# Kernel tuning notes

Hardware: AMD Instinct MI355X
Metric: run time of the kernel (lower is better)

The kernel has to match this reference:

```python
import jax, jax.numpy as jnp
import numpy as np

N_NODES = 100000
N_EDGES = 1600000
IN_CH, HID_CH, OUT_CH = 128, 128, 64
N_GRAPHS = 64


def gcn_conv(x, src, dst, W, b, n_nodes):
    """PyG-style GCNConv: self-loops already included in (src, dst).
    out_i = b + sum_j norm_ij * (x_j @ W), norm_ij = deg_i^-1/2 * deg_j^-1/2."""
    xw = x @ W  # [N, out]
    deg = jax.ops.segment_sum(jnp.ones_like(dst, dtype=xw.dtype), dst,
                              num_segments=n_nodes)  # [N]
    dinv = jnp.where(deg > 0, jax.lax.rsqrt(jnp.maximum(deg, 1e-12)), 0.0)
    norm = dinv[src] * dinv[dst]  # [E]
    msg = xw[src] * norm[:, None]  # gather + scale  [E, out]
    out = jax.ops.segment_sum(msg, dst, num_segments=n_nodes)  # scatter-add
    return out + b


def global_mean_pool(x, batch, n_graphs):
    s = jax.ops.segment_sum(x, batch, num_segments=n_graphs)
    cnt = jax.ops.segment_sum(jnp.ones((x.shape[0],), x.dtype), batch,
                              num_segments=n_graphs)
    return s / jnp.maximum(cnt, 1.0)[:, None]


def setup_inputs() -> dict:
    key = jax.random.key(0)
    ks = jax.random.split(key, 9)
    x = jax.random.normal(ks[0], (N_NODES, IN_CH), dtype=jnp.float32)
    edge_index = jax.random.randint(ks[1], (2, N_EDGES), 0, N_NODES, dtype=jnp.int64)
    batch = jnp.sort(jax.random.randint(ks[2], (N_NODES,), 0, N_GRAPHS, dtype=jnp.int64))
    # Glorot-ish params
    s1 = 1.0 / np.sqrt(IN_CH)
    s2 = 1.0 / np.sqrt(HID_CH)
    W1 = jax.random.normal(ks[3], (IN_CH, HID_CH), jnp.float32) * s1
    b1 = jnp.zeros((HID_CH,), jnp.float32)
    W2 = jax.random.normal(ks[4], (HID_CH, HID_CH), jnp.float32) * s2
    b2 = jnp.zeros((HID_CH,), jnp.float32)
    Wl = jax.random.normal(ks[5], (HID_CH, OUT_CH), jnp.float32) * s2
    bl = jax.random.normal(ks[6], (OUT_CH,), jnp.float32) * 0.01
    return {"x": x, "edge_index": edge_index, "batch": batch,
            "W1": W1, "b1": b1, "W2": W2, "b2": b2, "Wl": Wl, "bl": bl}


def reference(x, edge_index, batch, W1, b1, W2, b2, Wl, bl):
    n = x.shape[0]
    loop = jnp.arange(n, dtype=edge_index.dtype)
    src = jnp.concatenate([edge_index[0], loop])  # add self-loops
    dst = jnp.concatenate([edge_index[1], loop])
    h = jax.nn.relu(gcn_conv(x, src, dst, W1, b1, n))
    h = jax.nn.relu(gcn_conv(h, src, dst, W2, b2, n))
    g = global_mean_pool(h, batch, N_GRAPHS)  # [B, hid]
    return g @ Wl + bl  # [B, out]
```

## Files before the change

kernel.cpp:

```cpp
#include <hip/hip_runtime.h>

#define N_NODESC 100000
#define N_EDGESC 1600000
#define CH 128
#define NG 64
#define OC 64

#define GST_BLKS 391
#define MFMA_BLKS 1563
#define PAD_STRIDE 64
#define SENTINEL N_NODESC

#define BIN_SHIFT 9
#define BIN_W 512
#define NBINS 196
#define BIN_CAP 16384
#define BIN1_BLKS 391
#define E_PER_BIN1 4096

typedef __attribute__((ext_vector_type(8))) short short8;
typedef __attribute__((ext_vector_type(4))) float f32x4;

__device__ __forceinline__ unsigned short f2b_u(float f) {
    union { float f; unsigned int u; } x; x.f = f;
    unsigned int u = x.u;
    return (unsigned short)((u + 0x7fffu + ((u >> 16) & 1u)) >> 16);
}
__device__ __forceinline__ float b2f_lo(unsigned int v) {
    union { unsigned int u; float f; } x; x.u = v << 16; return x.f;
}
__device__ __forceinline__ float b2f_hi(unsigned int v) {
    union { unsigned int u; float f; } x; x.u = v & 0xffff0000u; return x.f;
}

#define WSTR 136
template<int AFP>
__device__ __forceinline__ void mfma_compute(int blk, int t, const void* __restrict__ Ap,
                                             unsigned short* __restrict__ Ob,
                                             const unsigned short* WsT) {
    int wave = t >> 6, lane = t & 63;
    int quad = lane >> 4, l16 = lane & 15;
    int arow = blk * 64 + wave * 16 + l16;
    bool rowok = arow < N_NODESC;
    f32x4 acc[8] = {};
#pragma unroll
    for (int c = 0; c < 4; ++c) {
        int koff = c * 32 + quad * 8;
        short8 a;
        if (AFP) {
            const float* A = (const float*)Ap;
            float4 f0 = make_float4(0, 0, 0, 0), f1 = make_float4(0, 0, 0, 0);
            if (rowok) {
                f0 = *(const float4*)(A + (size_t)arow * 128 + koff);
                f1 = *(const float4*)(A + (size_t)arow * 128 + koff + 4);
            }
            a[0] = (short)f2b_u(f0.x); a[1] = (short)f2b_u(f0.y);
            a[2] = (short)f2b_u(f0.z); a[3] = (short)f2b_u(f0.w);
            a[4] = (short)f2b_u(f1.x); a[5] = (short)f2b_u(f1.y);
            a[6] = (short)f2b_u(f1.z); a[7] = (short)f2b_u(f1.w);
        } else {
            const unsigned short* A = (const unsigned short*)Ap;
            if (rowok) a = *(const short8*)(A + (size_t)arow * 128 + koff);
            else       a = (short8)(short)0;
        }
#pragma unroll
        for (int tt = 0; tt < 8; ++tt) {
            short8 b = *(const short8*)&WsT[(tt * 16 + l16) * WSTR + koff];
            acc[tt] = __builtin_amdgcn_mfma_f32_16x16x32_bf16(a, b, acc[tt], 0, 0, 0);
        }
    }
    int orow0 = blk * 64 + wave * 16 + quad * 4;
#pragma unroll
    for (int r = 0; r < 4; ++r) {
        int g = orow0 + r;
        if (g < N_NODESC) {
#pragma unroll
            for (int tt = 0; tt < 8; ++tt)
                Ob[(size_t)g * 128 + tt * 16 + l16] = f2b_u(acc[tt][r]);
        }
    }
}

__global__ __launch_bounds__(256) void k_pre(const int* __restrict__ ei,
                                             const int* __restrict__ batch,
                                             const float* __restrict__ W1,
                                             const float* __restrict__ W2,
                                             int* __restrict__ cursor,
                                             unsigned int* __restrict__ binbuf,
                                             unsigned short* __restrict__ Wt1,
                                             unsigned short* __restrict__ Wt2,
                                             int* __restrict__ gstart) {
    __shared__ int hist[NBINS];
    int b = blockIdx.x, t = threadIdx.x;
    if (b < BIN1_BLKS) {
        for (int i = t; i < NBINS; i += 256) hist[i] = 0;
        __syncthreads();
        int e0 = b * E_PER_BIN1;
#pragma unroll 4
        for (int i = 0; i < E_PER_BIN1 / 256; ++i) {
            int e = e0 + i * 256 + t;
            if (e < N_EDGESC) atomicAdd(&hist[ei[N_EDGESC + e] >> BIN_SHIFT], 1);
        }
        __syncthreads();
        for (int i = t; i < NBINS; i += 256) {
            int c = hist[i];
            hist[i] = c ? atomicAdd(&cursor[i], c) : 0;
        }
        __syncthreads();
#pragma unroll 4
        for (int i = 0; i < E_PER_BIN1 / 256; ++i) {
            int e = e0 + i * 256 + t;
            if (e < N_EDGESC) {
                int d = ei[N_EDGESC + e];
                int s = ei[e];
                int bin = d >> BIN_SHIFT;
                int off = atomicAdd(&hist[bin], 1);
                binbuf[(size_t)bin * BIN_CAP + off] =
                    ((unsigned int)(d & (BIN_W - 1)) << 17) | (unsigned int)s;
            }
        }
    } else if (b < BIN1_BLKS + 64) {
        int i = (b - BIN1_BLKS) * 256 + t;
        int k = i >> 7, c = i & 127;
        Wt1[c * 128 + k] = f2b_u(W1[k * 128 + c]);
    } else if (b < BIN1_BLKS + 128) {
        int i = (b - BIN1_BLKS - 64) * 256 + t;
        int k = i >> 7, c = i & 127;
        Wt2[c * 128 + k] = f2b_u(W2[k * 128 + c]);
    } else {
        int i = (b - BIN1_BLKS - 128) * 256 + t;
        if (i >= N_NODESC) return;
        int bb = batch[i];
        int bp = (i == 0) ? -1 : batch[i - 1];
        for (int g = bp + 1; g <= bb; ++g) gstart[g] = i;
        if (i == N_NODESC - 1)
            for (int g = bb + 1; g <= NG; ++g) gstart[g] = N_NODESC;
    }
}

__global__ __launch_bounds__(256) void k_main(const float* __restrict__ x,
                                              const unsigned short* __restrict__ Wt1,
                                              unsigned short* __restrict__ xw,
                                              const int* __restrict__ cursor,
                                              const unsigned int* __restrict__ binbuf,
                                              int* __restrict__ deg,
                                              float* __restrict__ dinvt,
                                              int* __restrict__ pad) {
    __shared__ unsigned short WsT[128 * WSTR];
    int t = threadIdx.x;
    if (blockIdx.x < NBINS) {
        int bin = blockIdx.x;
        if (bin == 0 && t == 0) dinvt[SENTINEL] = 0.f;
        int* ldeg = (int*)WsT;
        for (int i = t; i < BIN_W; i += 256) ldeg[i] = 0;
        __syncthreads();
        int n = cursor[bin];
        size_t base = (size_t)bin * BIN_CAP;
        for (int i = t; i < n; i += 256) {
            unsigned int rec = binbuf[base + i];
            int dl = rec >> 17;
            int s = rec & 0x1FFFF;
            int slot = atomicAdd(&ldeg[dl], 1) & (PAD_STRIDE - 1);
            pad[(size_t)((bin << BIN_SHIFT) + dl) * PAD_STRIDE + slot] = s;
        }
        __syncthreads();
        for (int i = t; i < BIN_W; i += 256) {
            int node = (bin << BIN_SHIFT) + i;
            if (node < N_NODESC) {
                int dg = ldeg[i];
                if (dg > PAD_STRIDE) dg = PAD_STRIDE;
                deg[node] = dg;
                dinvt[node] = rsqrtf((float)(dg + 1));
                int r8 = (dg + 7) & ~7;
                for (int j = dg; j < r8; ++j)
                    pad[(size_t)node * PAD_STRIDE + j] = SENTINEL;
            }
        }
    } else {
        int blk = blockIdx.x - NBINS;
        const uint4* wsrc = (const uint4*)Wt1;
        for (int idx = t; idx < 2048; idx += 256) {
            int row = idx >> 4, sub = idx & 15;
            *((uint4*)&WsT[row * WSTR] + sub) = wsrc[row * 16 + sub];
        }
        __syncthreads();
        mfma_compute<1>(blk, t, x, xw, WsT);
    }
}

__global__ __launch_bounds__(256) void k_mfma2(const unsigned short* __restrict__ A,
                                               const unsigned short* __restrict__ Wt,
                                               unsigned short* __restrict__ Ob) {
    __shared__ unsigned short WsT[128 * WSTR];
    int t = threadIdx.x;
    {
        const uint4* wsrc = (const uint4*)Wt;
        for (int idx = t; idx < 2048; idx += 256) {
            int row = idx >> 4, sub = idx & 15;
            *((uint4*)&WsT[row * WSTR] + sub) = wsrc[row * 16 + sub];
        }
    }
    __syncthreads();
    mfma_compute<0>(blockIdx.x, t, A, Ob, WsT);
}

__device__ __forceinline__ void gather8(const unsigned int* __restrict__ xw,
                                        const int* __restrict__ pad,
                                        const float* __restrict__ dinvt,
                                        int base, int lane,
                                        float& acc0, float& acc1) {
    int s[8];
    float w[8];
    unsigned int v[8];
#pragma unroll
    for (int k = 0; k < 8; ++k) s[k] = pad[base + k];
#pragma unroll
    for (int k = 0; k < 8; ++k) {
        w[k] = dinvt[s[k]];
        v[k] = xw[(unsigned int)(s[k] * 64 + lane)];
    }
#pragma unroll
    for (int k = 0; k < 8; ++k) {
        acc0 += w[k] * b2f_lo(v[k]);
        acc1 += w[k] * b2f_hi(v[k]);
    }
}

__device__ __forceinline__ void gather_pair(const unsigned int* __restrict__ xw,
                                            const int* __restrict__ pad,
                                            const float* __restrict__ dinvt,
                                            int nA, int nB, int dgA, int dgB, int lane,
                                            float& a0, float& a1, float& b0, float& b1) {
    int ngA = (dgA + 7) >> 3, ngB = (dgB + 7) >> 3;
    int baseA = nA * PAD_STRIDE, baseB = nB * PAD_STRIDE;
    int ngmin = ngA < ngB ? ngA : ngB;
    int g = 0;
    for (; g < ngmin; ++g) {
        gather8(xw, pad, dinvt, baseA + g * 8, lane, a0, a1);
        gather8(xw, pad, dinvt, baseB + g * 8, lane, b0, b1);
    }
    for (; g < ngA; ++g) gather8(xw, pad, dinvt, baseA + g * 8, lane, a0, a1);
    for (; g < ngB; ++g) gather8(xw, pad, dinvt, baseB + g * 8, lane, b0, b1);
}

__global__ __launch_bounds__(256) void k_gather1(const unsigned int* __restrict__ xw,
                                                 const int* __restrict__ deg,
                                                 const float* __restrict__ dinvt,
                                                 const int* __restrict__ pad,
                                                 const float* __restrict__ bias,
                                                 unsigned int* __restrict__ outp) {
    int t = threadIdx.x;
    int lane = t & 63;
    int nA = blockIdx.x * 8 + (t >> 6) * 2;
    if (nA >= N_NODESC) return;
    int nB = nA + 1;
    if (nB >= N_NODESC) nB = nA;
    int dgA = deg[nA], dgB = deg[nB];
    float wA = dinvt[nA], wB = dinvt[nB];
    unsigned int vsA = xw[(unsigned int)(nA * 64 + lane)];
    unsigned int vsB = xw[(unsigned int)(nB * 64 + lane)];
    float a0 = wA * b2f_lo(vsA), a1 = wA * b2f_hi(vsA);
    float b0 = wB * b2f_lo(vsB), b1 = wB * b2f_hi(vsB);
    gather_pair(xw, pad, dinvt, nA, nB, dgA, dgB, lane, a0, a1, b0, b1);
    float2 bb = ((const float2*)bias)[lane];
    float oA0 = fmaxf(bb.x + wA * a0, 0.f), oA1 = fmaxf(bb.y + wA * a1, 0.f);
    float oB0 = fmaxf(bb.x + wB * b0, 0.f), oB1 = fmaxf(bb.y + wB * b1, 0.f);
    outp[(unsigned int)(nA * 64 + lane)] =
        ((unsigned int)f2b_u(oA1) << 16) | (unsigned int)f2b_u(oA0);
    outp[(unsigned int)(nB * 64 + lane)] =
        ((unsigned int)f2b_u(oB1) << 16) | (unsigned int)f2b_u(oB0);
}

__global__ __launch_bounds__(256) void k_gather_pool(const unsigned int* __restrict__ xw,
                                                     const int* __restrict__ deg,
                                                     const float* __restrict__ dinvt,
                                                     const int* __restrict__ pad,
                                                     const float* __restrict__ bias,
                                                     const int* __restrict__ batch,
                                                     float* __restrict__ gpart) {
    __shared__ float lds[4 * 128];
    int t = threadIdx.x, w = t >> 6, lane = t & 63;
    int base = blockIdx.x * 16;
    bool fast = batch[base] == batch[base + 15];
    float2 bv = ((const float2*)bias)[lane];
    float sum0 = 0.f, sum1 = 0.f;
#pragma unroll
    for (int p = 0; p < 2; ++p) {
        int nA = base + w * 4 + p * 2;
        int nB = nA + 1;
        int dgA = deg[nA], dgB = deg[nB];
        float wA = dinvt[nA], wB = dinvt[nB];
        unsigned int vsA = xw[(unsigned int)(nA * 64 + lane)];
        unsigned int vsB = xw[(unsigned int)(nB * 64 + lane)];
        float a0 = wA * b2f_lo(vsA), a1 = wA * b2f_hi(vsA);
        float b0 = wB * b2f_lo(vsB), b1 = wB * b2f_hi(vsB);
        gather_pair(xw, pad, dinvt, nA, nB, dgA, dgB, lane, a0, a1, b0, b1);
        float oA0 = fmaxf(bv.x + wA * a0, 0.f), oA1 = fmaxf(bv.y + wA * a1, 0.f);
        float oB0 = fmaxf(bv.x + wB * b0, 0.f), oB1 = fmaxf(bv.y + wB * b1, 0.f);
        if (fast) {
            sum0 += oA0 + oB0; sum1 += oA1 + oB1;
        } else {
            int gA = batch[nA], gB = batch[nB];
            atomicAdd(&gpart[gA * 128 + lane * 2], oA0);
            atomicAdd(&gpart[gA * 128 + lane * 2 + 1], oA1);
            atomicAdd(&gpart[gB * 128 + lane * 2], oB0);
            atomicAdd(&gpart[gB * 128 + lane * 2 + 1], oB1);
        }
    }
    if (fast) {
        lds[w * 128 + lane * 2] = sum0;
        lds[w * 128 + lane * 2 + 1] = sum1;
        __syncthreads();
        if (t < 128) {
            float v = lds[t] + lds[128 + t] + lds[256 + t] + lds[384 + t];
            atomicAdd(&gpart[batch[base] * 128 + t], v);
        }
    }
}

__global__ void k_final(const float* __restrict__ gpart, const int* __restrict__ gstart,
                        const float* __restrict__ Wl, const float* __restrict__ bl,
                        float* __restrict__ out) {
    __shared__ float gs[128];
    int b = blockIdx.x;
    int o = threadIdx.x;
    gs[o] = gpart[b * 128 + o];
    gs[o + 64] = gpart[b * 128 + 64 + o];
    __syncthreads();
    int cnt = gstart[b + 1] - gstart[b];
    float sc = 1.f / (float)(cnt > 0 ? cnt : 1);
    float sum = 0.f;
    for (int k = 0; k < 128; ++k) sum += gs[k] * Wl[k * 64 + o];
    out[b * 64 + o] = bl[o] + sc * sum;
}

extern "C" void kernel_launch(void* const* d_in, const int* in_sizes, int n_in,
                              void* d_out, int out_size, void* d_ws, size_t ws_size,
                              hipStream_t stream) {
    const float* x    = (const float*)d_in[0];
    const int*   ei   = (const int*)d_in[1];
    const int*   batch= (const int*)d_in[2];
    const float* W1   = (const float*)d_in[3];
    const float* b1   = (const float*)d_in[4];
    const float* W2   = (const float*)d_in[5];
    const float* b2   = (const float*)d_in[6];
    const float* Wl   = (const float*)d_in[7];
    const float* bl   = (const float*)d_in[8];
    float* out = (float*)d_out;

    char* ws = (char*)d_ws;
    unsigned short* xw_s = (unsigned short*)ws; ws += (size_t)(N_NODESC + 1) * CH * 2;
    unsigned short* h_b  = (unsigned short*)ws; ws += (size_t)N_NODESC * CH * 2;
    unsigned short* Wt1 = (unsigned short*)ws; ws += (size_t)CH * CH * 2;
    unsigned short* Wt2 = (unsigned short*)ws; ws += (size_t)CH * CH * 2;
    int*   cursor = (int*)ws;   ws += (size_t)NBINS * 4;
    float* gpart  = (float*)ws; ws += (size_t)NG * CH * 4;
    int*   deg    = (int*)ws;   ws += (size_t)N_NODESC * 4;
    float* dinvt  = (float*)ws; ws += (size_t)(N_NODESC + 1) * 4;
    int*   pad    = (int*)ws;   ws += (size_t)N_NODESC * PAD_STRIDE * 4;
    unsigned int* binbuf = (unsigned int*)ws; ws += (size_t)NBINS * BIN_CAP * 4;
    int*   gstart = (int*)ws;   ws += (NG + 8) * 4;

    hipMemsetAsync(cursor, 0, (size_t)NBINS * 4 + (size_t)NG * CH * 4, stream);

    k_pre<<<BIN1_BLKS + 128 + GST_BLKS, 256, 0, stream>>>(ei, batch, W1, W2,
        cursor, binbuf, Wt1, Wt2, gstart);
    k_main<<<NBINS + MFMA_BLKS, 256, 0, stream>>>(x, Wt1, xw_s, cursor, binbuf,
                                                  deg, dinvt, pad);

    k_gather1<<<(N_NODESC + 7) / 8, 256, 0, stream>>>((const unsigned int*)xw_s,
        deg, dinvt, pad, b1, (unsigned int*)h_b);
    k_mfma2<<<MFMA_BLKS, 256, 0, stream>>>(h_b, Wt2, xw_s);
    k_gather_pool<<<N_NODESC / 16, 256, 0, stream>>>((const unsigned int*)xw_s,
        deg, dinvt, pad, b2, batch, gpart);

    k_final<<<NG, 64, 0, stream>>>(gpart, gstart, Wl, bl, out);
}
```

Measured before the change: 310.6 us.

## Gather neighbor rows with 16-byte loads, four nodes per wavefront

Restructures both aggregation kernels so each wavefront handles four nodes, with 16 lanes per node each loading a uint4 (8 bf16 channels) per neighbor row, instead of one node pair per wave with 4-byte loads. Neighbor indices are read as int4 and processed four at a time, padded up to a multiple of four with the sentinel node. The sentinel row of xw is zeroed in k_pre so padded entries add nothing. The goal is wider memory transactions and more neighbor loads in flight. The cost is more registers, partial-wave waste on low-degree nodes, and shuffle reductions for pooling.

```diff
diff --git a/kernel.cpp b/kernel.cpp
--- a/kernel.cpp
+++ b/kernel.cpp
@@ -89,7 +89,8 @@
                                              unsigned int* __restrict__ binbuf,
                                              unsigned short* __restrict__ Wt1,
                                              unsigned short* __restrict__ Wt2,
-                                             int* __restrict__ gstart) {
+                                             int* __restrict__ gstart,
+                                             unsigned int* __restrict__ xw0) {
     __shared__ int hist[NBINS];
     int b = blockIdx.x, t = threadIdx.x;
     if (b < BIN1_BLKS) {
@@ -129,7 +130,11 @@
         Wt2[c * 128 + k] = f2b_u(W2[k * 128 + c]);
     } else {
         int i = (b - BIN1_BLKS - 128) * 256 + t;
-        if (i >= N_NODESC) return;
+        if (i >= N_NODESC) {
+            int z = i - N_NODESC;
+            if (z < CH / 2) xw0[(size_t)SENTINEL * (CH / 2) + z] = 0;
+            return;
+        }
         int bb = batch[i];
         int bp = (i == 0) ? -1 : batch[i - 1];
         for (int g = bp + 1; g <= bb; ++g) gstart[g] = i;
@@ -204,43 +209,29 @@
     mfma_compute<0>(blockIdx.x, t, A, Ob, WsT);
 }
 
-__device__ __forceinline__ void gather8(const unsigned int* __restrict__ xw,
-                                        const int* __restrict__ pad,
-                                        const float* __restrict__ dinvt,
-                                        int base, int lane,
-                                        float& acc0, float& acc1) {
-    int s[8];
-    float w[8];
-    unsigned int v[8];
-#pragma unroll
-    for (int k = 0; k < 8; ++k) s[k] = pad[base + k];
-#pragma unroll
-    for (int k = 0; k < 8; ++k) {
-        w[k] = dinvt[s[k]];
-        v[k] = xw[(unsigned int)(s[k] * 64 + lane)];
-    }
-#pragma unroll
-    for (int k = 0; k < 8; ++k) {
-        acc0 += w[k] * b2f_lo(v[k]);
-        acc1 += w[k] * b2f_hi(v[k]);
-    }
-}
-
-__device__ __forceinline__ void gather_pair(const unsigned int* __restrict__ xw,
+#define ACC4(vv, ww)                                                        \
+    acc[0] += ww * b2f_lo(vv.x); acc[1] += ww * b2f_hi(vv.x);               \
+    acc[2] += ww * b2f_lo(vv.y); acc[3] += ww * b2f_hi(vv.y);               \
+    acc[4] += ww * b2f_lo(vv.z); acc[5] += ww * b2f_hi(vv.z);               \
+    acc[6] += ww * b2f_lo(vv.w); acc[7] += ww * b2f_hi(vv.w);
+
+__device__ __forceinline__ void group_accum(const unsigned int* __restrict__ xw,
+                                            const float* __restrict__ dinvt,
                                             const int* __restrict__ pad,
-                                            const float* __restrict__ dinvt,
-                                            int nA, int nB, int dgA, int dgB, int lane,
-                                            float& a0, float& a1, float& b0, float& b1) {
-    int ngA = (dgA + 7) >> 3, ngB = (dgB + 7) >> 3;
-    int baseA = nA * PAD_STRIDE, baseB = nB * PAD_STRIDE;
-    int ngmin = ngA < ngB ? ngA : ngB;
-    int g = 0;
-    for (; g < ngmin; ++g) {
-        gather8(xw, pad, dinvt, baseA + g * 8, lane, a0, a1);
-        gather8(xw, pad, dinvt, baseB + g * 8, lane, b0, b1);
-    }
-    for (; g < ngA; ++g) gather8(xw, pad, dinvt, baseA + g * 8, lane, a0, a1);
-    for (; g < ngB; ++g) gather8(xw, pad, dinvt, baseB + g * 8, lane, b0, b1);
+                                            int base, int l16, int nb,
+                                            float* acc) {
+    for (int kb = 0; kb < nb; ++kb) {
+        int4 pv = *(const int4*)&pad[base + kb * 4];
+        float w0 = dinvt[pv.x], w1 = dinvt[pv.y], w2 = dinvt[pv.z], w3 = dinvt[pv.w];
+        uint4 v0 = *(const uint4*)&xw[(unsigned int)pv.x * 64 + l16 * 4];
+        uint4 v1 = *(const uint4*)&xw[(unsigned int)pv.y * 64 + l16 * 4];
+        uint4 v2 = *(const uint4*)&xw[(unsigned int)pv.z * 64 + l16 * 4];
+        uint4 v3 = *(const uint4*)&xw[(unsigned int)pv.w * 64 + l16 * 4];
+        ACC4(v0, w0)
+        ACC4(v1, w1)
+        ACC4(v2, w2)
+        ACC4(v3, w3)
+    }
 }
 
 __global__ __launch_bounds__(256) void k_gather1(const unsigned int* __restrict__ xw,
@@ -250,25 +241,34 @@
                                                  const float* __restrict__ bias,
                                                  unsigned int* __restrict__ outp) {
     int t = threadIdx.x;
-    int lane = t & 63;
-    int nA = blockIdx.x * 8 + (t >> 6) * 2;
-    if (nA >= N_NODESC) return;
-    int nB = nA + 1;
-    if (nB >= N_NODESC) nB = nA;
-    int dgA = deg[nA], dgB = deg[nB];
-    float wA = dinvt[nA], wB = dinvt[nB];
-    unsigned int vsA = xw[(unsigned int)(nA * 64 + lane)];
-    unsigned int vsB = xw[(unsigned int)(nB * 64 + lane)];
-    float a0 = wA * b2f_lo(vsA), a1 = wA * b2f_hi(vsA);
-    float b0 = wB * b2f_lo(vsB), b1 = wB * b2f_hi(vsB);
-    gather_pair(xw, pad, dinvt, nA, nB, dgA, dgB, lane, a0, a1, b0, b1);
-    float2 bb = ((const float2*)bias)[lane];
-    float oA0 = fmaxf(bb.x + wA * a0, 0.f), oA1 = fmaxf(bb.y + wA * a1, 0.f);
-    float oB0 = fmaxf(bb.x + wB * b0, 0.f), oB1 = fmaxf(bb.y + wB * b1, 0.f);
-    outp[(unsigned int)(nA * 64 + lane)] =
-        ((unsigned int)f2b_u(oA1) << 16) | (unsigned int)f2b_u(oA0);
-    outp[(unsigned int)(nB * 64 + lane)] =
-        ((unsigned int)f2b_u(oB1) << 16) | (unsigned int)f2b_u(oB0);
+    int lane = t & 63, w = t >> 6;
+    int g = lane >> 4, l16 = lane & 15;
+    int node = blockIdx.x * 16 + w * 4 + g;
+    int dg = deg[node];
+    float wn = dinvt[node];
+    uint4 vs = *(const uint4*)&xw[(unsigned int)node * 64 + l16 * 4];
+    float acc[8];
+    acc[0] = wn * b2f_lo(vs.x); acc[1] = wn * b2f_hi(vs.x);
+    acc[2] = wn * b2f_lo(vs.y); acc[3] = wn * b2f_hi(vs.y);
+    acc[4] = wn * b2f_lo(vs.z); acc[5] = wn * b2f_hi(vs.z);
+    acc[6] = wn * b2f_lo(vs.w); acc[7] = wn * b2f_hi(vs.w);
+    group_accum(xw, dinvt, pad, node * PAD_STRIDE, l16, (dg + 3) >> 2, acc);
+    float4 bA = *(const float4*)&bias[l16 * 8];
+    float4 bB = *(const float4*)&bias[l16 * 8 + 4];
+    float o0 = fmaxf(bA.x + wn * acc[0], 0.f);
+    float o1 = fmaxf(bA.y + wn * acc[1], 0.f);
+    float o2 = fmaxf(bA.z + wn * acc[2], 0.f);
+    float o3 = fmaxf(bA.w + wn * acc[3], 0.f);
+    float o4 = fmaxf(bB.x + wn * acc[4], 0.f);
+    float o5 = fmaxf(bB.y + wn * acc[5], 0.f);
+    float o6 = fmaxf(bB.z + wn * acc[6], 0.f);
+    float o7 = fmaxf(bB.w + wn * acc[7], 0.f);
+    uint4 ov;
+    ov.x = ((unsigned int)f2b_u(o1) << 16) | (unsigned int)f2b_u(o0);
+    ov.y = ((unsigned int)f2b_u(o3) << 16) | (unsigned int)f2b_u(o2);
+    ov.z = ((unsigned int)f2b_u(o5) << 16) | (unsigned int)f2b_u(o4);
+    ov.w = ((unsigned int)f2b_u(o7) << 16) | (unsigned int)f2b_u(o6);
+    *(uint4*)&outp[(unsigned int)node * 64 + l16 * 4] = ov;
 }
 
 __global__ __launch_bounds__(256) void k_gather_pool(const unsigned int* __restrict__ xw,
@@ -280,41 +280,52 @@
                                                      float* __restrict__ gpart) {
     __shared__ float lds[4 * 128];
     int t = threadIdx.x, w = t >> 6, lane = t & 63;
+    int g = lane >> 4, l16 = lane & 15;
     int base = blockIdx.x * 16;
+    int node = base + w * 4 + g;
+    int dg = deg[node];
+    float wn = dinvt[node];
+    uint4 vs = *(const uint4*)&xw[(unsigned int)node * 64 + l16 * 4];
+    float acc[8];
+    acc[0] = wn * b2f_lo(vs.x); acc[1] = wn * b2f_hi(vs.x);
+    acc[2] = wn * b2f_lo(vs.y); acc[3] = wn * b2f_hi(vs.y);
+    acc[4] = wn * b2f_lo(vs.z); acc[5] = wn * b2f_hi(vs.z);
+    acc[6] = wn * b2f_lo(vs.w); acc[7] = wn * b2f_hi(vs.w);
+    group_accum(xw, dinvt, pad, node * PAD_STRIDE, l16, (dg + 3) >> 2, acc);
+    float4 bA = *(const float4*)&bias[l16 * 8];
+    float4 bB = *(const float4*)&bias[l16 * 8 + 4];
+    float o[8];
+    o[0] = fmaxf(bA.x + wn * acc[0], 0.f);
+    o[1] = fmaxf(bA.y + wn * acc[1], 0.f);
+    o[2] = fmaxf(bA.z + wn * acc[2], 0.f);
+    o[3] = fmaxf(bA.w + wn * acc[3], 0.f);
+    o[4] = fmaxf(bB.x + wn * acc[4], 0.f);
+    o[5] = fmaxf(bB.y + wn * acc[5], 0.f);
+    o[6] = fmaxf(bB.z + wn * acc[6], 0.f);
+    o[7] = fmaxf(bB.w + wn * acc[7], 0.f);
     bool fast = batch[base] == batch[base + 15];
-    float2 bv = ((const float2*)bias)[lane];
-    float sum0 = 0.f, sum1 = 0.f;
-#pragma unroll
-    for (int p = 0; p < 2; ++p) {
-        int nA = base + w * 4 + p * 2;
-        int nB = nA + 1;
-        int dgA = deg[nA], dgB = deg[nB];
-        float wA = dinvt[nA], wB = dinvt[nB];
-        unsigned int vsA = xw[(unsigned int)(nA * 64 + lane)];
-        unsigned int vsB = xw[(unsigned int)(nB * 64 + lane)];
-        float a0 = wA * b2f_lo(vsA), a1 = wA * b2f_hi(vsA);
-        float b0 = wB * b2f_lo(vsB), b1 = wB * b2f_hi(vsB);
-        gather_pair(xw, pad, dinvt, nA, nB, dgA, dgB, lane, a0, a1, b0, b1);
-        float oA0 = fmaxf(bv.x + wA * a0, 0.f), oA1 = fmaxf(bv.y + wA * a1, 0.f);
-        float oB0 = fmaxf(bv.x + wB * b0, 0.f), oB1 = fmaxf(bv.y + wB * b1, 0.f);
-        if (fast) {
-            sum0 += oA0 + oB0; sum1 += oA1 + oB1;
-        } else {
-            int gA = batch[nA], gB = batch[nB];
-            atomicAdd(&gpart[gA * 128 + lane * 2], oA0);
-            atomicAdd(&gpart[gA * 128 + lane * 2 + 1], oA1);
-            atomicAdd(&gpart[gB * 128 + lane * 2], oB0);
-            atomicAdd(&gpart[gB * 128 + lane * 2 + 1], oB1);
-        }
-    }
     if (fast) {
-        lds[w * 128 + lane * 2] = sum0;
-        lds[w * 128 + lane * 2 + 1] = sum1;
+#pragma unroll
+        for (int j = 0; j < 8; ++j) {
+            float v = o[j];
+            v += __shfl_xor(v, 16);
+            v += __shfl_xor(v, 32);
+            o[j] = v;
+        }
+        if (lane < 16) {
+#pragma unroll
+            for (int j = 0; j < 8; ++j) lds[w * 128 + l16 * 8 + j] = o[j];
+        }
         __syncthreads();
         if (t < 128) {
             float v = lds[t] + lds[128 + t] + lds[256 + t] + lds[384 + t];
             atomicAdd(&gpart[batch[base] * 128 + t], v);
         }
+    } else {
+        int gb = batch[node];
+#pragma unroll
+        for (int j = 0; j < 8; ++j)
+            atomicAdd(&gpart[gb * 128 + l16 * 8 + j], o[j]);
     }
 }
 
@@ -364,11 +375,11 @@
     hipMemsetAsync(cursor, 0, (size_t)NBINS * 4 + (size_t)NG * CH * 4, stream);
 
     k_pre<<<BIN1_BLKS + 128 + GST_BLKS, 256, 0, stream>>>(ei, batch, W1, W2,
-        cursor, binbuf, Wt1, Wt2, gstart);
+        cursor, binbuf, Wt1, Wt2, gstart, (unsigned int*)xw_s);
     k_main<<<NBINS + MFMA_BLKS, 256, 0, stream>>>(x, Wt1, xw_s, cursor, binbuf,
                                                   deg, dinvt, pad);
 
-    k_gather1<<<(N_NODESC + 7) / 8, 256, 0, stream>>>((const unsigned int*)xw_s,
+    k_gather1<<<N_NODESC / 16, 256, 0, stream>>>((const unsigned int*)xw_s,
         deg, dinvt, pad, b1, (unsigned int*)h_b);
     k_mfma2<<<MFMA_BLKS, 256, 0, stream>>>(h_b, Wt2, xw_s);
     k_gather_pool<<<N_NODESC / 16, 256, 0, stream>>>((const unsigned int*)xw_s,
```

New measurement: 306.2 us. About the same (-1.4%).
